# Kernel tuning notes

Measured on AMD Instinct MI355X. Metric: run time of the kernel, lower is better.

The kernel has to match this reference:

```python
import jax, jax.numpy as jnp
import numpy as np

D_MODEL, NHEAD = 1024, 16
DK = D_MODEL // NHEAD


def setup_inputs() -> dict:
    key = jax.random.key(0)
    ks = jax.random.split(key, 10)
    B, T = 2, 2048
    s = 1.0 / np.sqrt(D_MODEL)
    inp = {
        "x": jax.random.normal(ks[0], (B, T, D_MODEL), dtype=jnp.float32),
        "attn_bias": jax.random.normal(ks[1], (1, NHEAD, T, T), dtype=jnp.float32),
        "Wq": jax.random.normal(ks[2], (D_MODEL, D_MODEL), dtype=jnp.float32) * s,
        "bq": jnp.zeros((D_MODEL,), dtype=jnp.float32),
        "Wk": jax.random.normal(ks[3], (D_MODEL, D_MODEL), dtype=jnp.float32) * s,
        "bk": jnp.zeros((D_MODEL,), dtype=jnp.float32),
        "Wv": jax.random.normal(ks[4], (D_MODEL, D_MODEL), dtype=jnp.float32) * s,
        "bv": jnp.zeros((D_MODEL,), dtype=jnp.float32),
        "Wo": jax.random.normal(ks[5], (D_MODEL, D_MODEL), dtype=jnp.float32) * s,
        "bo": jnp.zeros((D_MODEL,), dtype=jnp.float32),
    }
    return inp


def reference(x, attn_bias, Wq, bq, Wk, bk, Wv, bv, Wo, bo):
    B, T, D = x.shape
    H, dk = NHEAD, DK
    # torch Linear: y = x @ W.T + b
    q = (x @ Wq.T + bq).reshape(B, T, H, dk).transpose(0, 2, 1, 3)  # [B,H,T,dk]
    k = (x @ Wk.T + bk).reshape(B, T, H, dk).transpose(0, 2, 1, 3)
    v = (x @ Wv.T + bv).reshape(B, T, H, dk).transpose(0, 2, 1, 3)
    scores = jnp.einsum("bhqd,bhkd->bhqk", q, k) / jnp.sqrt(jnp.float32(dk))
    scores = scores + attn_bias  # broadcast over batch
    attn = jax.nn.softmax(scores, axis=-1)  # dropout p=0.0 -> identity
    out = jnp.einsum("bhqk,bhkd->bhqd", attn, v)
    out = out.transpose(0, 2, 1, 3).reshape(B, T, D)
    return out @ Wo.T + bo
```

## Files before the change

kernel.cpp:

```cpp
#include <hip/hip_runtime.h>

typedef unsigned short u16;
typedef unsigned int u32;
using short8 = __attribute__((ext_vector_type(8))) short;
using f32x4  = __attribute__((ext_vector_type(4))) float;

#define D_MODEL 1024
#define NHEAD 16
#define DKV 64
#define TSEQ 2048
#define BATCH 2
#define L2E 1.44269504f
#define CSHIFT 12.0f

#define GLOAD16(gp, lp)                                                      \
    __builtin_amdgcn_global_load_lds(                                        \
        (const __attribute__((address_space(1))) u32*)(gp),                  \
        (__attribute__((address_space(3))) u32*)(lp), 16, 0, 0)

__device__ __forceinline__ u16 f2bf(float f) {
    union { float f; u32 i; } c; c.f = f;
    u32 x = c.i;
    return (u16)((x + 0x7FFFu + ((x >> 16) & 1u)) >> 16);
}
__device__ __forceinline__ u16 f2bf_fast(float f) {
    union { float f; u32 i; } c; c.f = f;
    return (u16)((c.i + 0x8000u) >> 16);
}

__global__ __launch_bounds__(256) void prep_cvt(
    const float* __restrict__ x,  const float* __restrict__ Wq,
    const float* __restrict__ Wk, const float* __restrict__ Wv,
    const float* __restrict__ Wo, u16* __restrict__ dst)
{
    size_t e = ((size_t)blockIdx.x * 256 + threadIdx.x) * 8;
    const float* src; size_t off;
    if (e < 4194304u)      { src = x;  off = e; }
    else if (e < 5242880u) { src = Wq; off = e - 4194304u; }
    else if (e < 6291456u) { src = Wk; off = e - 5242880u; }
    else if (e < 7340032u) { src = Wv; off = e - 6291456u; }
    else                   { src = Wo; off = e - 7340032u; }
    float4 a = *(const float4*)(src + off);
    float4 b = *(const float4*)(src + off + 4);
    short8 v;
    v[0] = (short)f2bf(a.x); v[1] = (short)f2bf(a.y);
    v[2] = (short)f2bf(a.z); v[3] = (short)f2bf(a.w);
    v[4] = (short)f2bf(b.x); v[5] = (short)f2bf(b.y);
    v[6] = (short)f2bf(b.z); v[7] = (short)f2bf(b.w);
    *(short8*)(dst + e) = v;
}

__global__ __launch_bounds__(256) void qkv_gemm(
    const u16* __restrict__ xbf, const u16* __restrict__ wbf,
    const float* __restrict__ bq, const float* __restrict__ bk,
    const float* __restrict__ bv, u16* __restrict__ qkv)
{
    __shared__ __align__(16) u16 Alds[128 * 64];
    __shared__ __align__(16) u16 Blds[128 * 64];

    const int fid = blockIdx.x;
    const int xcd = fid & 7, ii = fid >> 3;
    const int z = ii >> 5, r2 = ii & 31;
    const int nb = r2 & 7, mb = xcd * 4 + (r2 >> 3);
    const int n0 = nb * 128, m0 = mb * 128;
    const u16* W = wbf + (size_t)z * 1048576;
    const float* bias = (z == 0) ? bq : (z == 1) ? bk : bv;
    u16* out = qkv + (size_t)z * 4194304;

    const int t = threadIdx.x;
    const int wave = t >> 6, lane = t & 63, l15 = lane & 15, quad = lane >> 4;
    const int wm = (wave >> 1) * 64, wn = (wave & 1) * 64;

    f32x4 acc[4][4];
#pragma unroll
    for (int i = 0; i < 4; ++i)
#pragma unroll
        for (int j = 0; j < 4; ++j)
#pragma unroll
            for (int r = 0; r < 4; ++r) acc[i][j][r] = 0.f;

    const int rs = t >> 3, cs = (t & 7) * 8;
    const u16* ga = xbf + (size_t)(m0 + rs) * 1024 + cs;
    const u16* gb = W   + (size_t)(n0 + rs) * 1024 + cs;
    u16* la = &Alds[rs * 64 + cs];
    u16* lb = &Blds[rs * 64 + cs];

    for (int kt = 0; kt < 16; ++kt) {
        const int k0 = kt * 64;
#pragma unroll
        for (int c = 0; c < 4; ++c) {
            GLOAD16(ga + (size_t)(c * 32) * 1024 + k0, la + c * 32 * 64);
            GLOAD16(gb + (size_t)(c * 32) * 1024 + k0, lb + c * 32 * 64);
        }
        __syncthreads();
#pragma unroll
        for (int ki = 0; ki < 2; ++ki) {
            short8 af[4], bfr[4];
#pragma unroll
            for (int i = 0; i < 4; ++i)
                af[i] = *(const short8*)&Alds[(wm + i * 16 + l15) * 64 + ki * 32 + quad * 8];
#pragma unroll
            for (int j = 0; j < 4; ++j)
                bfr[j] = *(const short8*)&Blds[(wn + j * 16 + l15) * 64 + ki * 32 + quad * 8];
#pragma unroll
            for (int i = 0; i < 4; ++i)
#pragma unroll
                for (int j = 0; j < 4; ++j)
                    acc[i][j] = __builtin_amdgcn_mfma_f32_16x16x32_bf16(af[i], bfr[j], acc[i][j], 0, 0, 0);
        }
        __syncthreads();
    }

#pragma unroll
    for (int j = 0; j < 4; ++j) {
        int n = n0 + wn + j * 16 + l15;
        float bb = bias[n];
        int h = n >> 6, d = n & 63;
#pragma unroll
        for (int i = 0; i < 4; ++i)
#pragma unroll
            for (int r = 0; r < 4; ++r) {
                int m = m0 + wm + i * 16 + quad * 4 + r;
                int bidx = m >> 11, tt = m & 2047;
                out[(((size_t)(bidx * NHEAD + h)) * TSEQ + tt) * DKV + d] =
                    f2bf(acc[i][j][r] + bb);
            }
    }
}

__global__ __launch_bounds__(512, 4) void attn_kernel(
    const u16* __restrict__ qws, const u16* __restrict__ kws, const u16* __restrict__ vws,
    const float* __restrict__ bias, u16* __restrict__ ows)
{
    __shared__ __align__(16) u16 Klds[2][64 * 64];
    __shared__ __align__(16) u16 Vt[2][2][64 * 72];
    __shared__ __align__(16) u16 Plds[2][64 * 72];

    const int fid = blockIdx.x;
    const int xcd = fid & 7, ii = fid >> 3;
    const int h = xcd * 2 + (ii >> 5);
    const int qt = ii & 31;
    const int q0 = qt * 64;

    const int t = threadIdx.x;
    const int bg = t >> 8;
    const int tl = t & 255;
    const int wave = tl >> 6, lane = tl & 63, l15 = lane & 15, quad = lane >> 4;
    const int bh = bg * NHEAD + h;
    const size_t bhoff = (size_t)bh * TSEQ * DKV;

    short8 qa0, qa1;
    {
        const u16* qp = qws + bhoff + (size_t)(q0 + wave * 16 + l15) * DKV;
        qa0 = *(const short8*)(qp + quad * 8);
        qa1 = *(const short8*)(qp + 32 + quad * 8);
    }

    float l_run[4] = {0.f, 0.f, 0.f, 0.f};
    f32x4 o_acc[4];
#pragma unroll
    for (int db = 0; db < 4; ++db)
#pragma unroll
        for (int r = 0; r < 4; ++r) o_acc[db][r] = 0.f;

    const float* bias_h = bias + ((size_t)h * TSEQ + q0) * TSEQ;
    const int a8 = tl & 7, c8 = a8 * 8, rp = tl >> 3;
    const int rbase = wave * 16 + quad * 4;
    const int sw8 = l15 & 7;

    const u16* kpbase = kws + bhoff + (size_t)rp * DKV + ((a8 ^ (rp & 7)) * 8);
    u16* kl = &Klds[bg][rp * 64 + c8];

    for (int kt = 0; kt < TSEQ / 64; ++kt) {
        const int kc0 = kt * 64;
        u16* vtb = &Vt[bg][kt & 1][0];

        float bz[16];
#pragma unroll
        for (int cb = 0; cb < 4; ++cb)
#pragma unroll
            for (int r = 0; r < 4; ++r)
                bz[cb * 4 + r] =
                    bias_h[(size_t)(rbase + r) * TSEQ + kc0 + cb * 16 + l15];

        {
            const u16* kp = kpbase + (size_t)kc0 * DKV;
            GLOAD16(kp, kl);
            GLOAD16(kp + 32 * DKV, kl + 32 * 64);
        }
        {
            const u16* vp = vws + bhoff + (size_t)(kc0 + 2 * rp) * DKV + c8;
            short8 v0 = *(const short8*)vp;
            short8 v1 = *(const short8*)(vp + DKV);
            int bk = rp >> 2;
            int kcl = (2 * rp) & 7;
#pragma unroll
            for (int j = 0; j < 8; ++j) {
                int d = c8 + j;
                u32 val = ((u32)(u16)v0[j]) | (((u32)(u16)v1[j]) << 16);
                *(u32*)&vtb[d * 72 + ((bk ^ a8) * 8) + kcl] = val;
            }
        }
        __syncthreads();

        f32x4 s[4];
#pragma unroll
        for (int cb = 0; cb < 4; ++cb)
#pragma unroll
            for (int r = 0; r < 4; ++r) s[cb][r] = 0.f;
#pragma unroll
        for (int cb = 0; cb < 4; ++cb) {
            const u16* kr = &Klds[bg][(cb * 16 + l15) * 64];
            short8 kb0 = *(const short8*)(kr + ((quad ^ sw8) * 8));
            short8 kb1 = *(const short8*)(kr + (((quad + 4) ^ sw8) * 8));
            s[cb] = __builtin_amdgcn_mfma_f32_16x16x32_bf16(qa0, kb0, s[cb], 0, 0, 0);
            s[cb] = __builtin_amdgcn_mfma_f32_16x16x32_bf16(qa1, kb1, s[cb], 0, 0, 0);
        }

#pragma unroll
        for (int cb = 0; cb < 4; ++cb)
#pragma unroll
            for (int r = 0; r < 4; ++r) {
                float arg = fmaf(s[cb][r], 0.125f * L2E,
                                 fmaf(bz[cb * 4 + r], L2E, -CSHIFT * L2E));
                float p = exp2f(arg);
                l_run[r] += p;
                Plds[bg][(rbase + r) * 72 + cb * 16 + l15] = f2bf_fast(p);
            }
        __syncthreads();

        {
            const u16* pr = &Plds[bg][(wave * 16 + l15) * 72 + quad * 8];
            short8 pa0 = *(const short8*)pr;
            short8 pa1 = *(const short8*)(pr + 32);
#pragma unroll
            for (int db = 0; db < 4; ++db) {
                int d = db * 16 + l15;
                int sw = (d >> 3) & 7;
                const u16* vr = &vtb[d * 72];
                short8 vb0 = *(const short8*)(vr + ((quad ^ sw) * 8));
                short8 vb1 = *(const short8*)(vr + (((4 + quad) ^ sw) * 8));
                o_acc[db] = __builtin_amdgcn_mfma_f32_16x16x32_bf16(pa0, vb0, o_acc[db], 0, 0, 0);
                o_acc[db] = __builtin_amdgcn_mfma_f32_16x16x32_bf16(pa1, vb1, o_acc[db], 0, 0, 0);
            }
        }
    }

#pragma unroll
    for (int r = 0; r < 4; ++r) {
        float v = l_run[r];
        v += __shfl_xor(v, 1);
        v += __shfl_xor(v, 2);
        v += __shfl_xor(v, 4);
        v += __shfl_xor(v, 8);
        l_run[r] = v;
    }
#pragma unroll
    for (int r = 0; r < 4; ++r) {
        float inv = 1.f / l_run[r];
        int row = q0 + rbase + r;
#pragma unroll
        for (int db = 0; db < 4; ++db)
            ows[bhoff + (size_t)row * DKV + db * 16 + l15] = f2bf(o_acc[db][r] * inv);
    }
}

__global__ __launch_bounds__(256) void out_gemm(
    const u16* __restrict__ ows, const u16* __restrict__ wobf,
    const float* __restrict__ bo, float* __restrict__ out)
{
    __shared__ __align__(16) u16 Alds[128 * 64];
    __shared__ __align__(16) u16 Blds[64 * 64];

    const int fid = blockIdx.x;
    const int xcd = fid & 7, ii = fid >> 3;
    const int nb = ii & 15, mb = xcd * 4 + (ii >> 4);
    const int n0 = nb * 64, m0 = mb * 128;

    const int t = threadIdx.x;
    const int wave = t >> 6, lane = t & 63, l15 = lane & 15, quad = lane >> 4;
    const int wm = (wave >> 1) * 64, wn = (wave & 1) * 32;

    f32x4 acc[4][2];
#pragma unroll
    for (int i = 0; i < 4; ++i)
#pragma unroll
        for (int j = 0; j < 2; ++j)
#pragma unroll
            for (int r = 0; r < 4; ++r) acc[i][j][r] = 0.f;

    const int rs = t >> 3, cs = (t & 7) * 8;
    const int bidx = m0 >> 11, tt0 = m0 & 2047;
    const u16* gaBase = ows + (((size_t)(bidx * NHEAD)) * TSEQ + tt0 + rs) * DKV + cs;
    const u16* gb = wobf + (size_t)(n0 + rs) * 1024 + cs;
    u16* la = &Alds[rs * 64 + cs];
    u16* lb = &Blds[rs * 64 + cs];

    for (int kt = 0; kt < 16; ++kt) {
        const int k0 = kt * 64;
#pragma unroll
        for (int c = 0; c < 4; ++c)
            GLOAD16(gaBase + ((size_t)kt * TSEQ + c * 32) * DKV, la + c * 32 * 64);
#pragma unroll
        for (int c = 0; c < 2; ++c)
            GLOAD16(gb + (size_t)(c * 32) * 1024 + k0, lb + c * 32 * 64);
        __syncthreads();
#pragma unroll
        for (int ki = 0; ki < 2; ++ki) {
            short8 af[4], bfr[2];
#pragma unroll
            for (int i = 0; i < 4; ++i)
                af[i] = *(const short8*)&Alds[(wm + i * 16 + l15) * 64 + ki * 32 + quad * 8];
#pragma unroll
            for (int j = 0; j < 2; ++j)
                bfr[j] = *(const short8*)&Blds[(wn + j * 16 + l15) * 64 + ki * 32 + quad * 8];
#pragma unroll
            for (int i = 0; i < 4; ++i)
#pragma unroll
                for (int j = 0; j < 2; ++j)
                    acc[i][j] = __builtin_amdgcn_mfma_f32_16x16x32_bf16(af[i], bfr[j], acc[i][j], 0, 0, 0);
        }
        __syncthreads();
    }

#pragma unroll
    for (int j = 0; j < 2; ++j) {
        int n = n0 + wn + j * 16 + l15;
        float bb = bo[n];
#pragma unroll
        for (int i = 0; i < 4; ++i)
#pragma unroll
            for (int r = 0; r < 4; ++r) {
                int m = m0 + wm + i * 16 + quad * 4 + r;
                out[(size_t)m * 1024 + n] = acc[i][j][r] + bb;
            }
    }
}

extern "C" void kernel_launch(void* const* d_in, const int* in_sizes, int n_in,
                              void* d_out, int out_size, void* d_ws, size_t ws_size,
                              hipStream_t stream)
{
    const float* x  = (const float*)d_in[0];
    const float* ab = (const float*)d_in[1];
    const float* Wq = (const float*)d_in[2];
    const float* bq = (const float*)d_in[3];
    const float* Wk = (const float*)d_in[4];
    const float* bk = (const float*)d_in[5];
    const float* Wv = (const float*)d_in[6];
    const float* bv = (const float*)d_in[7];
    const float* Wo = (const float*)d_in[8];
    const float* bo = (const float*)d_in[9];
    float* out = (float*)d_out;

    u16* wsu = (u16*)d_ws;
    const size_t WBF = 4194304;
    const size_t QKV = 8388608;
    const size_t OWS = 20971520;
    const size_t QSZ = 4194304;

    prep_cvt<<<4096, 256, 0, stream>>>(x, Wq, Wk, Wv, Wo, wsu);
    qkv_gemm<<<768, 256, 0, stream>>>(wsu, wsu + WBF, bq, bk, bv, wsu + QKV);
    attn_kernel<<<512, 512, 0, stream>>>(wsu + QKV, wsu + QKV + QSZ,
                                         wsu + QKV + 2 * QSZ, ab, wsu + OWS);
    out_gemm<<<512, 256, 0, stream>>>(wsu + OWS, wsu + WBF + 3 * 1048576, bo, out);
}
```

Measured before the change: 501.8 us.

## Double-buffer K/V tiles with prefetch and drop the mid-loop barrier

K and V for the next key tile are now loaded into alternate LDS buffers while the current tile is computed, with a prologue loading the first tile. This leaves one __syncthreads per iteration instead of two. The P buffer drops its padded 72 stride for a 64 stride with XOR swizzling. Because each wave only reads back its own P rows, the barrier between the P write and the PV matmul is removed. The cost is more LDS for the double-buffered K and a redundant reload of the final tile, plus reliance on wave-local LDS ordering.

```diff
diff --git a/kernel.cpp b/kernel.cpp
--- a/kernel.cpp
+++ b/kernel.cpp
@@ -132,9 +132,9 @@
     const u16* __restrict__ qws, const u16* __restrict__ kws, const u16* __restrict__ vws,
     const float* __restrict__ bias, u16* __restrict__ ows)
 {
-    __shared__ __align__(16) u16 Klds[2][64 * 64];
-    __shared__ __align__(16) u16 Vt[2][2][64 * 72];
-    __shared__ __align__(16) u16 Plds[2][64 * 72];
+    __shared__ __align__(16) u16 Klds[2][2][64 * 64];
+    __shared__ __align__(16) u16 Vt[2][2][64 * 64];
+    __shared__ __align__(16) u16 Plds[2][64 * 64];
 
     const int fid = blockIdx.x;
     const int xcd = fid & 7, ii = fid >> 3;
@@ -167,13 +167,41 @@
     const int a8 = tl & 7, c8 = a8 * 8, rp = tl >> 3;
     const int rbase = wave * 16 + quad * 4;
     const int sw8 = l15 & 7;
+    const int vbk = rp >> 2;
+    const int vsl = 2 * (rp & 3);
 
     const u16* kpbase = kws + bhoff + (size_t)rp * DKV + ((a8 ^ (rp & 7)) * 8);
-    u16* kl = &Klds[bg][rp * 64 + c8];
+    const u16* vpbase = vws + bhoff + (size_t)(2 * rp) * DKV + c8;
+    u16* klA = &Klds[bg][0][rp * 64 + c8];
+    u16* klB = &Klds[bg][1][rp * 64 + c8];
+
+    {
+        GLOAD16(kpbase, klA);
+        GLOAD16(kpbase + 32 * DKV, klA + 32 * 64);
+        short8 v0 = *(const short8*)vpbase;
+        short8 v1 = *(const short8*)(vpbase + DKV);
+        u16* vtb = &Vt[bg][0][0];
+#pragma unroll
+        for (int j = 0; j < 8; ++j) {
+            int d = c8 + j;
+            u32 val = ((u32)(u16)v0[j]) | (((u32)(u16)v1[j]) << 16);
+            *(u32*)&vtb[d * 64 + ((vbk ^ a8) * 8) + vsl] = val;
+        }
+    }
+    __syncthreads();
 
     for (int kt = 0; kt < TSEQ / 64; ++kt) {
         const int kc0 = kt * 64;
-        u16* vtb = &Vt[bg][kt & 1][0];
+        const int cur = kt & 1;
+
+        const size_t koff = (size_t)((kt < 31) ? kc0 + 64 : kc0) * DKV;
+        {
+            u16* kl = cur ? klA : klB;
+            GLOAD16(kpbase + koff, kl);
+            GLOAD16(kpbase + koff + 32 * DKV, kl + 32 * 64);
+        }
+        short8 v0n = *(const short8*)(vpbase + koff);
+        short8 v1n = *(const short8*)(vpbase + koff + DKV);
 
         float bz[16];
 #pragma unroll
@@ -183,26 +211,6 @@
                 bz[cb * 4 + r] =
                     bias_h[(size_t)(rbase + r) * TSEQ + kc0 + cb * 16 + l15];
 
-        {
-            const u16* kp = kpbase + (size_t)kc0 * DKV;
-            GLOAD16(kp, kl);
-            GLOAD16(kp + 32 * DKV, kl + 32 * 64);
-        }
-        {
-            const u16* vp = vws + bhoff + (size_t)(kc0 + 2 * rp) * DKV + c8;
-            short8 v0 = *(const short8*)vp;
-            short8 v1 = *(const short8*)(vp + DKV);
-            int bk = rp >> 2;
-            int kcl = (2 * rp) & 7;
-#pragma unroll
-            for (int j = 0; j < 8; ++j) {
-                int d = c8 + j;
-                u32 val = ((u32)(u16)v0[j]) | (((u32)(u16)v1[j]) << 16);
-                *(u32*)&vtb[d * 72 + ((bk ^ a8) * 8) + kcl] = val;
-            }
-        }
-        __syncthreads();
-
         f32x4 s[4];
 #pragma unroll
         for (int cb = 0; cb < 4; ++cb)
@@ -210,7 +218,7 @@
             for (int r = 0; r < 4; ++r) s[cb][r] = 0.f;
 #pragma unroll
         for (int cb = 0; cb < 4; ++cb) {
-            const u16* kr = &Klds[bg][(cb * 16 + l15) * 64];
+            const u16* kr = &Klds[bg][cur][(cb * 16 + l15) * 64];
             short8 kb0 = *(const short8*)(kr + ((quad ^ sw8) * 8));
             short8 kb1 = *(const short8*)(kr + (((quad + 4) ^ sw8) * 8));
             s[cb] = __builtin_amdgcn_mfma_f32_16x16x32_bf16(qa0, kb0, s[cb], 0, 0, 0);
@@ -225,25 +233,40 @@
                                  fmaf(bz[cb * 4 + r], L2E, -CSHIFT * L2E));
                 float p = exp2f(arg);
                 l_run[r] += p;
-                Plds[bg][(rbase + r) * 72 + cb * 16 + l15] = f2bf_fast(p);
-            }
-        __syncthreads();
+                int row = rbase + r;
+                int chunk = cb * 2 + (l15 >> 3);
+                Plds[bg][row * 64 + ((chunk ^ (row & 7)) * 8) + (l15 & 7)] =
+                    f2bf_fast(p);
+            }
 
         {
-            const u16* pr = &Plds[bg][(wave * 16 + l15) * 72 + quad * 8];
-            short8 pa0 = *(const short8*)pr;
-            short8 pa1 = *(const short8*)(pr + 32);
+            const int prow = wave * 16 + l15;
+            const u16* prb = &Plds[bg][prow * 64];
+            short8 pa0 = *(const short8*)(prb + ((quad ^ sw8) * 8));
+            short8 pa1 = *(const short8*)(prb + (((quad + 4) ^ sw8) * 8));
+            const u16* vtc = &Vt[bg][cur][0];
 #pragma unroll
             for (int db = 0; db < 4; ++db) {
                 int d = db * 16 + l15;
                 int sw = (d >> 3) & 7;
-                const u16* vr = &vtb[d * 72];
+                const u16* vr = &vtc[d * 64];
                 short8 vb0 = *(const short8*)(vr + ((quad ^ sw) * 8));
                 short8 vb1 = *(const short8*)(vr + (((4 + quad) ^ sw) * 8));
                 o_acc[db] = __builtin_amdgcn_mfma_f32_16x16x32_bf16(pa0, vb0, o_acc[db], 0, 0, 0);
                 o_acc[db] = __builtin_amdgcn_mfma_f32_16x16x32_bf16(pa1, vb1, o_acc[db], 0, 0, 0);
             }
         }
+
+        {
+            u16* vtb = &Vt[bg][cur ^ 1][0];
+#pragma unroll
+            for (int j = 0; j < 8; ++j) {
+                int d = c8 + j;
+                u32 val = ((u32)(u16)v0n[j]) | (((u32)(u16)v1n[j]) << 16);
+                *(u32*)&vtb[d * 64 + ((vbk ^ a8) * 8) + vsl] = val;
+            }
+        }
+        __syncthreads();
     }
 
 #pragma unroll
```

Measured after the change: 605.5 us. 1.21x slower.

## Software-pipeline K, V and bias loads one tile ahead in attention loop

Applied to the files above, without the earlier changes.

Restructures the attention key-tile loop so the next tile's K (via global_load_lds), V and attention-bias values are issued right after the current QK MFMAs. They are then consumed in the following iteration, with V staged into the alternate half of the double-buffered transposed V LDS. This is meant to hide global-memory latency, especially the large fp32 bias stream, behind the softmax and PV MFMA work. It also drops the barrier between the P write and the PV read, relying on each wave reading only its own P rows. The cost is extra registers for the prefetched values, which may reduce occupancy, plus a redundant reload on the last iteration.

```diff
diff --git a/kernel.cpp b/kernel.cpp
--- a/kernel.cpp
+++ b/kernel.cpp
@@ -167,41 +167,36 @@
     const int a8 = tl & 7, c8 = a8 * 8, rp = tl >> 3;
     const int rbase = wave * 16 + quad * 4;
     const int sw8 = l15 & 7;
+    const int vbk = rp >> 2;
+    const int vkcl = (2 * rp) & 7;
 
     const u16* kpbase = kws + bhoff + (size_t)rp * DKV + ((a8 ^ (rp & 7)) * 8);
+    const u16* vpbase = vws + bhoff + (size_t)(2 * rp) * DKV + c8;
     u16* kl = &Klds[bg][rp * 64 + c8];
 
+    GLOAD16(kpbase, kl);
+    GLOAD16(kpbase + 32 * DKV, kl + 32 * 64);
+    {
+        short8 v0 = *(const short8*)vpbase;
+        short8 v1 = *(const short8*)(vpbase + DKV);
+        u16* vtb = &Vt[bg][0][0];
+#pragma unroll
+        for (int j = 0; j < 8; ++j) {
+            int d = c8 + j;
+            u32 val = ((u32)(u16)v0[j]) | (((u32)(u16)v1[j]) << 16);
+            *(u32*)&vtb[d * 72 + ((vbk ^ a8) * 8) + vkcl] = val;
+        }
+    }
+    float bz[16];
+#pragma unroll
+    for (int cb = 0; cb < 4; ++cb)
+#pragma unroll
+        for (int r = 0; r < 4; ++r)
+            bz[cb * 4 + r] = bias_h[(size_t)(rbase + r) * TSEQ + cb * 16 + l15];
+    __syncthreads();
+
     for (int kt = 0; kt < TSEQ / 64; ++kt) {
-        const int kc0 = kt * 64;
-        u16* vtb = &Vt[bg][kt & 1][0];
-
-        float bz[16];
-#pragma unroll
-        for (int cb = 0; cb < 4; ++cb)
-#pragma unroll
-            for (int r = 0; r < 4; ++r)
-                bz[cb * 4 + r] =
-                    bias_h[(size_t)(rbase + r) * TSEQ + kc0 + cb * 16 + l15];
-
-        {
-            const u16* kp = kpbase + (size_t)kc0 * DKV;
-            GLOAD16(kp, kl);
-            GLOAD16(kp + 32 * DKV, kl + 32 * 64);
-        }
-        {
-            const u16* vp = vws + bhoff + (size_t)(kc0 + 2 * rp) * DKV + c8;
-            short8 v0 = *(const short8*)vp;
-            short8 v1 = *(const short8*)(vp + DKV);
-            int bk = rp >> 2;
-            int kcl = (2 * rp) & 7;
-#pragma unroll
-            for (int j = 0; j < 8; ++j) {
-                int d = c8 + j;
-                u32 val = ((u32)(u16)v0[j]) | (((u32)(u16)v1[j]) << 16);
-                *(u32*)&vtb[d * 72 + ((bk ^ a8) * 8) + kcl] = val;
-            }
-        }
-        __syncthreads();
+        const int cur = kt & 1;
 
         f32x4 s[4];
 #pragma unroll
@@ -217,6 +212,22 @@
             s[cb] = __builtin_amdgcn_mfma_f32_16x16x32_bf16(qa1, kb1, s[cb], 0, 0, 0);
         }
 
+        __syncthreads();
+
+        const int ktn = (kt < 31) ? kt + 1 : kt;
+        const size_t koff = (size_t)ktn * 64 * DKV;
+        GLOAD16(kpbase + koff, kl);
+        GLOAD16(kpbase + koff + 32 * DKV, kl + 32 * 64);
+        short8 v0n = *(const short8*)(vpbase + koff);
+        short8 v1n = *(const short8*)(vpbase + koff + DKV);
+        float bzn[16];
+#pragma unroll
+        for (int cb = 0; cb < 4; ++cb)
+#pragma unroll
+            for (int r = 0; r < 4; ++r)
+                bzn[cb * 4 + r] =
+                    bias_h[(size_t)(rbase + r) * TSEQ + ktn * 64 + cb * 16 + l15];
+
 #pragma unroll
         for (int cb = 0; cb < 4; ++cb)
 #pragma unroll
@@ -227,23 +238,37 @@
                 l_run[r] += p;
                 Plds[bg][(rbase + r) * 72 + cb * 16 + l15] = f2bf_fast(p);
             }
-        __syncthreads();
 
         {
             const u16* pr = &Plds[bg][(wave * 16 + l15) * 72 + quad * 8];
             short8 pa0 = *(const short8*)pr;
             short8 pa1 = *(const short8*)(pr + 32);
+            const u16* vtc = &Vt[bg][cur][0];
 #pragma unroll
             for (int db = 0; db < 4; ++db) {
                 int d = db * 16 + l15;
                 int sw = (d >> 3) & 7;
-                const u16* vr = &vtb[d * 72];
+                const u16* vr = &vtc[d * 72];
                 short8 vb0 = *(const short8*)(vr + ((quad ^ sw) * 8));
                 short8 vb1 = *(const short8*)(vr + (((4 + quad) ^ sw) * 8));
                 o_acc[db] = __builtin_amdgcn_mfma_f32_16x16x32_bf16(pa0, vb0, o_acc[db], 0, 0, 0);
                 o_acc[db] = __builtin_amdgcn_mfma_f32_16x16x32_bf16(pa1, vb1, o_acc[db], 0, 0, 0);
             }
         }
+
+        {
+            u16* vtb = &Vt[bg][cur ^ 1][0];
+#pragma unroll
+            for (int j = 0; j < 8; ++j) {
+                int d = c8 + j;
+                u32 val = ((u32)(u16)v0n[j]) | (((u32)(u16)v1n[j]) << 16);
+                *(u32*)&vtb[d * 72 + ((vbk ^ a8) * 8) + vkcl] = val;
+            }
+        }
+#pragma unroll
+        for (int i = 0; i < 16; ++i) bz[i] = bzn[i];
+
+        __syncthreads();
     }
 
 #pragma unroll
```

Result: no change. 505.5 us (+0.7%).
